# Kernel optimization log

Measured on AMD Instinct MI355X. Metric: run time of the kernel, lower is better.

The kernel has to match this reference:

```python
import jax, jax.numpy as jnp
import numpy as np

N_NODES = 50000
N_EDGES = 800000
D_IN = 256
D_OUT = 128


def setup_inputs() -> dict:
    key = jax.random.key(0)
    k1, k2, k3 = jax.random.split(key, 3)
    x = jax.random.normal(k1, (N_NODES, D_IN), dtype=jnp.float32)
    edge_index = jax.random.randint(k2, (2, N_EDGES), 0, N_NODES, dtype=jnp.int64)
    W = jax.random.normal(k3, (D_IN, D_OUT), dtype=jnp.float32) / np.sqrt(D_IN)
    b = jnp.zeros((D_OUT,), dtype=jnp.float32)
    prelu_a = jnp.full((D_OUT,), 0.25, dtype=jnp.float32)  # PyTorch PReLU default init
    return {"x": x, "edge_index": edge_index, "W": W, "b": b, "prelu_a": prelu_a}


def reference(x, edge_index, W, b, prelu_a):
    N = x.shape[0]
    # GCNConv default: add self-loops, symmetric deg^{-1/2} normalization
    self_loops = jnp.arange(N, dtype=edge_index.dtype)
    src = jnp.concatenate([edge_index[0], self_loops])  # message source j
    dst = jnp.concatenate([edge_index[1], self_loops])  # aggregation target i
    deg = jax.ops.segment_sum(jnp.ones_like(dst, dtype=x.dtype), dst, num_segments=N)
    dinv = jnp.where(deg > 0, jax.lax.rsqrt(deg), 0.0)
    norm = dinv[src] * dinv[dst]  # [E+N]
    h = x @ W  # [N, D_OUT] linear transform before aggregation
    msg = h[src] * norm[:, None]  # gather + scale
    out = jax.ops.segment_sum(msg, dst, num_segments=N) + b  # scatter-add + bias
    # per-channel PReLU
    return jnp.where(out > 0, out, prelu_a * out)
```

## Files before the change

kernel.cpp:

```cpp
#include <hip/hip_runtime.h>

#define N_NODES 50000
#define N_EDGES 800000
#define D_IN    256
#define D_OUT   128
#define ELL_S   64
#define PART_BLKS 391
#define PACK_BLKS 16
#define GEMM_BLKS 391
#define NBINS   196
#define EPB     2048
#define CAPB    40

typedef __attribute__((ext_vector_type(8))) short short8;
typedef __attribute__((ext_vector_type(4))) float floatx4;

__device__ __forceinline__ unsigned short f2bf(float f) {
    unsigned int u = __float_as_uint(f);
    unsigned int r = (u + 0x7fffu + ((u >> 16) & 1u)) >> 16;
    return (unsigned short)r;
}
__device__ __forceinline__ unsigned int pack2(float a, float b) {
    return (unsigned int)f2bf(a) | ((unsigned int)f2bf(b) << 16);
}
__device__ __forceinline__ float bfl(unsigned int u) { return __uint_as_float(u << 16); }
__device__ __forceinline__ float bfh(unsigned int u) { return __uint_as_float(u & 0xffff0000u); }

__global__ __launch_bounds__(256) void part_kernel(const void* __restrict__ ei,
                                                   const float* __restrict__ W,
                                                   unsigned short* __restrict__ bfrag,
                                                   int* __restrict__ packed,
                                                   int* __restrict__ blkBinCnt) {
    __shared__ int hist[NBINS];
    __shared__ int found32;
    const int bid = blockIdx.x;
    const int tid = threadIdx.x;

    if (bid >= PART_BLKS) {
        int g = (bid - PART_BLKS) * 256 + tid;
        int gl = g & 63;
        int kc = (g >> 6) & 7;
        int ct = g >> 9;
        int n  = ct * 16 + (gl & 15);
        int kb = kc * 32 + ((gl >> 4) & 3) * 8;
        unsigned int p[4];
#pragma unroll
        for (int jj = 0; jj < 4; jj++) {
            float a = W[(size_t)(kb + 2 * jj + 0) * D_OUT + n];
            float b = W[(size_t)(kb + 2 * jj + 1) * D_OUT + n];
            p[jj] = pack2(a, b);
        }
        *(uint4*)&bfrag[(size_t)g * 8] = make_uint4(p[0], p[1], p[2], p[3]);
        return;
    }

    int sb = bid;
    if (tid < NBINS) hist[tid] = 0;
    if (tid == 0) found32 = 0;
    __syncthreads();
    {
        const unsigned int* e32 = (const unsigned int*)ei;
        if (e32[2 * tid + 1] != 0u) atomicOr(&found32, 1);
    }
    __syncthreads();
    int is64 = !found32;

    int ebase = sb * EPB + tid;
    int sv[8], bn[8], dl[8], lr[8];
    if (is64) {
        const long long* p = (const long long*)ei;
#pragma unroll
        for (int i = 0; i < 8; i++) {
            int e = ebase + i * 256;
            if (e < N_EDGES) {
                sv[i] = (int)p[e];
                int d = (int)p[N_EDGES + e];
                bn[i] = d >> 8; dl[i] = d & 255;
            } else bn[i] = -1;
        }
    } else {
        const int* p = (const int*)ei;
#pragma unroll
        for (int i = 0; i < 8; i++) {
            int e = ebase + i * 256;
            if (e < N_EDGES) {
                sv[i] = p[e];
                int d = p[N_EDGES + e];
                bn[i] = d >> 8; dl[i] = d & 255;
            } else bn[i] = -1;
        }
    }
#pragma unroll
    for (int i = 0; i < 8; i++)
        if (bn[i] >= 0) lr[i] = atomicAdd(&hist[bn[i]], 1);
#pragma unroll
    for (int i = 0; i < 8; i++) {
        if (bn[i] >= 0 && lr[i] < CAPB)
            packed[((size_t)sb * NBINS + bn[i]) * CAPB + lr[i]] = sv[i] | (dl[i] << 24);
    }
    __syncthreads();
    for (int t = tid; t < NBINS; t += 256)
        blkBinCnt[sb * NBINS + t] = hist[t];
}

__global__ __launch_bounds__(256) void fused_kernel(const float* __restrict__ x,
                                                    const unsigned short* __restrict__ bf,
                                                    unsigned short* __restrict__ h,
                                                    const int* __restrict__ packed,
                                                    const int* __restrict__ blkBinCnt,
                                                    int* __restrict__ cnt,
                                                    int* __restrict__ bucket) {
    __shared__ unsigned short As[128][40];
    __shared__ int c256[256];
    int tid = threadIdx.x;

    if (blockIdx.x >= GEMM_BLKS) {
        int j = blockIdx.x - GEMM_BLKS;
        c256[tid] = 0;
        __syncthreads();
        for (int sb = tid; sb < PART_BLKS; sb += 256) {
            int c = blkBinCnt[sb * NBINS + j];
            if (c > CAPB) c = CAPB;
            const int* seg = packed + ((size_t)sb * NBINS + j) * CAPB;
            for (int r = 0; r < c; ++r) {
                int rec = seg[r];
                int dl  = ((unsigned int)rec) >> 24;
                int s   = rec & 0xFFFFFF;
                int pos = atomicAdd(&c256[dl], 1);
                if (pos < ELL_S) bucket[(size_t)((j << 8) + dl) * ELL_S + pos] = s;
            }
        }
        __syncthreads();
        int d = (j << 8) + tid;
        if (d < N_NODES) cnt[d] = c256[tid];
        return;
    }

    int row0 = blockIdx.x * 128;
    int w    = tid >> 6;
    int lane = tid & 63;
    int quad = lane >> 4;
    int l15  = lane & 15;

    floatx4 acc[2][8];
#pragma unroll
    for (int i = 0; i < 2; i++)
#pragma unroll
        for (int j = 0; j < 8; j++) acc[i][j] = (floatx4){0.f, 0.f, 0.f, 0.f};

    int srow  = tid >> 1;
    int shalf = (tid & 1) * 16;
    const float* xrow = x + (size_t)(row0 + srow) * D_IN;
    bool svalid = (row0 + srow) < N_NODES;

    for (int k0 = 0; k0 < D_IN; k0 += 32) {
        uint4 p0 = make_uint4(0, 0, 0, 0), p1 = make_uint4(0, 0, 0, 0);
        if (svalid) {
            const float* src = xrow + k0 + shalf;
            float4 f0 = *(const float4*)(src + 0);
            float4 f1 = *(const float4*)(src + 4);
            float4 f2 = *(const float4*)(src + 8);
            float4 f3 = *(const float4*)(src + 12);
            p0 = make_uint4(pack2(f0.x, f0.y), pack2(f0.z, f0.w),
                            pack2(f1.x, f1.y), pack2(f1.z, f1.w));
            p1 = make_uint4(pack2(f2.x, f2.y), pack2(f2.z, f2.w),
                            pack2(f3.x, f3.y), pack2(f3.z, f3.w));
        }
        __syncthreads();
        *(uint4*)&As[srow][shalf + 0] = p0;
        *(uint4*)&As[srow][shalf + 8] = p1;
        __syncthreads();

        short8 a0 = *(const short8*)&As[w * 32 + l15][quad * 8];
        short8 a1 = *(const short8*)&As[w * 32 + 16 + l15][quad * 8];
        int kc = k0 >> 5;
#pragma unroll
        for (int ct = 0; ct < 8; ct++) {
            short8 b = *(const short8*)&bf[(size_t)(((ct * 8 + kc) * 64 + lane)) * 8];
            acc[0][ct] = __builtin_amdgcn_mfma_f32_16x16x32_bf16(a0, b, acc[0][ct], 0, 0, 0);
            acc[1][ct] = __builtin_amdgcn_mfma_f32_16x16x32_bf16(a1, b, acc[1][ct], 0, 0, 0);
        }
    }

#pragma unroll
    for (int rt = 0; rt < 2; rt++) {
        int grow0 = row0 + w * 32 + rt * 16 + quad * 4;
#pragma unroll
        for (int r = 0; r < 4; r++) {
            int grow = grow0 + r;
            if (grow < N_NODES) {
#pragma unroll
                for (int ct = 0; ct < 8; ct++) {
                    h[(size_t)grow * D_OUT + ct * 16 + l15] = f2bf(acc[rt][ct][r]);
                }
            }
        }
    }
}

#define GACC(U, F)                                      \
    a0 += bfl(U.x) * (F); a1 += bfh(U.x) * (F);         \
    a2 += bfl(U.y) * (F); a3 += bfh(U.y) * (F);         \
    a4 += bfl(U.z) * (F); a5 += bfh(U.z) * (F);         \
    a6 += bfl(U.w) * (F); a7 += bfh(U.w) * (F);

#define GBODY(SS, WW, KB)                                                         \
    {                                                                             \
        int lim = n - (KB);                                                       \
        if (lim > 16) lim = 16;                                                   \
        lim = (lim + 3) & ~3;                                                     \
        for (int k = 0; k < lim; k += 4) {                                        \
            int   s0 = __shfl((SS), gk + k + 0), s1 = __shfl((SS), gk + k + 1);   \
            int   s2 = __shfl((SS), gk + k + 2), s3 = __shfl((SS), gk + k + 3);   \
            float f0 = __shfl((WW), gk + k + 0), f1 = __shfl((WW), gk + k + 1);   \
            float f2 = __shfl((WW), gk + k + 2), f3 = __shfl((WW), gk + k + 3);   \
            uint4 u0 = *(const uint4*)(h + (size_t)s0 * D_OUT + co);              \
            uint4 u1 = *(const uint4*)(h + (size_t)s1 * D_OUT + co);              \
            uint4 u2 = *(const uint4*)(h + (size_t)s2 * D_OUT + co);              \
            uint4 u3 = *(const uint4*)(h + (size_t)s3 * D_OUT + co);              \
            GACC(u0, f0); GACC(u1, f1); GACC(u2, f2); GACC(u3, f3);               \
        }                                                                         \
    }

__global__ __launch_bounds__(256) void gather_kernel(
    const unsigned short* __restrict__ h, const int* __restrict__ cnt,
    const int* __restrict__ bucket, const float* __restrict__ bias,
    const float* __restrict__ pa, float* __restrict__ out) {
    int wave = (int)((blockIdx.x * blockDim.x + threadIdx.x) >> 6);
    int lane = threadIdx.x & 63;
    int g  = lane >> 4;
    int l  = lane & 15;
    int gk = g << 4;
    int d  = wave * 4 + g;
    if (wave >= N_NODES / 4) return;

    int nraw = cnt[d];
    int n = nraw < ELL_S ? nraw : ELL_S;
    if (n < 0) n = 0;
    float di = rsqrtf((float)(nraw + 1));

    int co = l * 8;

    uint4 us = *(const uint4*)(h + (size_t)d * D_OUT + co);
    float sl = di * di;
    float a0 = bfl(us.x) * sl, a1 = bfh(us.x) * sl;
    float a2 = bfl(us.y) * sl, a3 = bfh(us.y) * sl;
    float a4 = bfl(us.z) * sl, a5 = bfh(us.z) * sl;
    float a6 = bfl(us.w) * sl, a7 = bfh(us.w) * sl;

    int db = d * ELL_S;
    int   s0v = 0,   s1v = 0,   s2v = 0,   s3v = 0;
    float w0v = 0.f, w1v = 0.f, w2v = 0.f, w3v = 0.f;
    if (l      < n) { s0v = bucket[db + l];      w0v = rsqrtf((float)(cnt[s0v] + 1)) * di; }
    if (l + 16 < n) { s1v = bucket[db + l + 16]; w1v = rsqrtf((float)(cnt[s1v] + 1)) * di; }
    if (l + 32 < n) { s2v = bucket[db + l + 32]; w2v = rsqrtf((float)(cnt[s2v] + 1)) * di; }
    if (l + 48 < n) { s3v = bucket[db + l + 48]; w3v = rsqrtf((float)(cnt[s3v] + 1)) * di; }

    if (n > 0)  GBODY(s0v, w0v, 0)
    if (n > 16) GBODY(s1v, w1v, 16)
    if (n > 32) GBODY(s2v, w2v, 32)
    if (n > 48) GBODY(s3v, w3v, 48)

    int c = l * 8;
    float4 b0 = *(const float4*)&bias[c];
    float4 b1 = *(const float4*)&bias[c + 4];
    float4 p0 = *(const float4*)&pa[c];
    float4 p1 = *(const float4*)&pa[c + 4];
    float4 o0, o1;
    o0.x = a0 + b0.x; o0.y = a1 + b0.y; o0.z = a2 + b0.z; o0.w = a3 + b0.w;
    o1.x = a4 + b1.x; o1.y = a5 + b1.y; o1.z = a6 + b1.z; o1.w = a7 + b1.w;
    o0.x = o0.x > 0.f ? o0.x : p0.x * o0.x;
    o0.y = o0.y > 0.f ? o0.y : p0.y * o0.y;
    o0.z = o0.z > 0.f ? o0.z : p0.z * o0.z;
    o0.w = o0.w > 0.f ? o0.w : p0.w * o0.w;
    o1.x = o1.x > 0.f ? o1.x : p1.x * o1.x;
    o1.y = o1.y > 0.f ? o1.y : p1.y * o1.y;
    o1.z = o1.z > 0.f ? o1.z : p1.z * o1.z;
    o1.w = o1.w > 0.f ? o1.w : p1.w * o1.w;
    *(float4*)&out[(size_t)d * D_OUT + c]     = o0;
    *(float4*)&out[(size_t)d * D_OUT + c + 4] = o1;
}

extern "C" void kernel_launch(void* const* d_in, const int* in_sizes, int n_in,
                              void* d_out, int out_size, void* d_ws, size_t ws_size,
                              hipStream_t stream) {
    const float* x  = (const float*)d_in[0];
    const void*  ei = d_in[1];
    const float* W  = (const float*)d_in[2];
    const float* b  = (const float*)d_in[3];
    const float* pa = (const float*)d_in[4];
    float* out = (float*)d_out;

    char* w = (char*)d_ws;
    unsigned short* bfrag = (unsigned short*)w; w += 8 * 8 * 64 * 8 * 2;
    int*   packed = (int*)w;    w += (size_t)PART_BLKS * NBINS * CAPB * 4;
    int*   bbc    = (int*)w;    w += (size_t)PART_BLKS * NBINS * 4;
    int*   cnt    = (int*)w;    w += (size_t)NBINS * 256 * 4;
    int*   bucket = (int*)w;    w += (size_t)N_NODES * ELL_S * 4;
    unsigned short* h = (unsigned short*)w; w += (size_t)N_NODES * D_OUT * 2;

    part_kernel<<<PART_BLKS + PACK_BLKS, 256, 0, stream>>>(ei, W, bfrag, packed, bbc);
    fused_kernel<<<GEMM_BLKS + NBINS, 256, 0, stream>>>(x, bfrag, h, packed, bbc, cnt, bucket);
    gather_kernel<<<(N_NODES / 4 * 64 + 255) / 256, 256, 0, stream>>>(h, cnt, bucket, b, pa, out);
}
```

Baseline: 172.8 us.

## Sort bucket neighbor lists by source tile via two-pass counting

The bucket-fill path now counts each destination's incoming edges per source-index tile (s>>13) in a first pass, prefix-sums those counts, then re-reads the packed records to place sources in tile-sorted order. Grouping neighbors by source range is meant to improve locality of the later h gathers in the aggregation. In exchange it reads the packed records twice and uses a larger shared histogram, which adds cost to the bucketing blocks.

```diff
diff --git a/kernel.cpp b/kernel.cpp
--- a/kernel.cpp
+++ b/kernel.cpp
@@ -11,6 +11,7 @@
 #define NBINS   196
 #define EPB     2048
 #define CAPB    40
+#define NTILE   8
 
 typedef __attribute__((ext_vector_type(8))) short short8;
 typedef __attribute__((ext_vector_type(4))) float floatx4;
@@ -111,12 +112,13 @@
                                                     int* __restrict__ cnt,
                                                     int* __restrict__ bucket) {
     __shared__ unsigned short As[128][40];
-    __shared__ int c256[256];
+    __shared__ unsigned int hcnt[256][NTILE];
     int tid = threadIdx.x;
 
     if (blockIdx.x >= GEMM_BLKS) {
         int j = blockIdx.x - GEMM_BLKS;
-        c256[tid] = 0;
+#pragma unroll
+        for (int t = 0; t < NTILE; t++) hcnt[tid][t] = 0;
         __syncthreads();
         for (int sb = tid; sb < PART_BLKS; sb += 256) {
             int c = blkBinCnt[sb * NBINS + j];
@@ -126,13 +128,34 @@
                 int rec = seg[r];
                 int dl  = ((unsigned int)rec) >> 24;
                 int s   = rec & 0xFFFFFF;
-                int pos = atomicAdd(&c256[dl], 1);
+                atomicAdd(&hcnt[dl][s >> 13], 1u);
+            }
+        }
+        __syncthreads();
+        {
+            unsigned int run = 0;
+#pragma unroll
+            for (int t = 0; t < NTILE; t++) {
+                unsigned int c = hcnt[tid][t];
+                hcnt[tid][t] = run;
+                run += c;
+            }
+            int d = (j << 8) + tid;
+            if (d < N_NODES) cnt[d] = (int)run;
+        }
+        __syncthreads();
+        for (int sb = tid; sb < PART_BLKS; sb += 256) {
+            int c = blkBinCnt[sb * NBINS + j];
+            if (c > CAPB) c = CAPB;
+            const int* seg = packed + ((size_t)sb * NBINS + j) * CAPB;
+            for (int r = 0; r < c; ++r) {
+                int rec = seg[r];
+                int dl  = ((unsigned int)rec) >> 24;
+                int s   = rec & 0xFFFFFF;
+                unsigned int pos = atomicAdd(&hcnt[dl][s >> 13], 1u);
                 if (pos < ELL_S) bucket[(size_t)((j << 8) + dl) * ELL_S + pos] = s;
             }
         }
-        __syncthreads();
-        int d = (j << 8) + tid;
-        if (d < N_NODES) cnt[d] = c256[tid];
         return;
     }
 
```

New measurement: 172.0 us. No clear change (-0.4%).
